# Performance work log

Hardware: AMD Instinct MI355X
Metric: run time of the kernel (lower is better)

The kernel has to match this reference:

```python
import jax, jax.numpy as jnp
import numpy as np

KERNEL_SIZE = 5
SMOOTH_NR = 0.0
SMOOTH_DR = 1e-05


def _box_mean(x, k):
    # Depthwise 3D box (mean) filter via three separable 1-D convolutions.
    # x: [B, C, H, W, D]; zero padding 'SAME' matches F.conv3d(padding=(k-1)//2).
    C = x.shape[1]
    pad = (k - 1) // 2
    for axis in range(3):
        kshape = [1, 1, 1]
        kshape[axis] = k
        kern = jnp.full((C, 1) + tuple(kshape), 1.0 / k, dtype=x.dtype)
        padding = [(pad, pad) if i == axis else (0, 0) for i in range(3)]
        x = jax.lax.conv_general_dilated(
            x, kern, window_strides=(1, 1, 1), padding=padding,
            feature_group_count=C,
            dimension_numbers=('NCDHW', 'OIDHW', 'NCDHW'))
    return x


def setup_inputs() -> dict:
    key = jax.random.key(0)
    k1, k2 = jax.random.split(key)
    shape = (2, 1, 192, 192, 192)
    pred = jax.random.normal(k1, shape, dtype=jnp.float32)
    target = jax.random.normal(k2, shape, dtype=jnp.float32)
    return {"pred": pred, "target": target}


def reference(pred, target):
    k = KERNEL_SIZE
    # Local (windowed) means of the 5 intermediates: I, J, I^2, J^2, I*J.
    # Stack into a single 5C-channel tensor like ffo.create_intermediates,
    # then one grouped box filter (as in the original conv3d with groups=5C).
    C = pred.shape[1]
    interm = jnp.concatenate(
        [pred, target, pred * pred, target * target, pred * target], axis=1)
    m = _box_mean(interm, k)
    uI, uJ, I2, J2, IJ = jnp.split(m, 5, axis=1)
    cross = IJ - uI * uJ          # local covariance (mean form)
    var_i = I2 - uI * uI          # local variance of pred
    var_j = J2 - uJ * uJ          # local variance of target
    ncc = (cross * cross + SMOOTH_NR) / (var_i * var_j + SMOOTH_DR)
    # reduction='mean'; loss is negative squared local NCC
    return -jnp.mean(ncc)
```

## Files before the change

### kernel.cpp

```cpp
#include <hip/hip_runtime.h>

#define HH 192
#define WW 192
#define DD 192
#define BB 2
#define WWDD (WW * DD)
#define HCHUNK 40
#define NSLAB 5
#define SLICES (HCHUNK + 4)

#define QROW 272
#define QSIZE (20 * QROW)
#define IJOFF QSIZE
#define IJROW 72
#define BUFSZ (QSIZE + 20 * IJROW)
#define LDS_BYTES (2 * BUFSZ)

__global__ __launch_bounds__(256, 6)
void lncc_fused_kernel(const float* __restrict__ pred,
                       const float* __restrict__ targ,
                       double* __restrict__ acc_out) {
    __shared__ alignas(16) char lds[LDS_BYTES];
    __shared__ float wpart[4];

    const int tx = threadIdx.x, ty = threadIdx.y;
    const int tid = ty * 16 + tx;

    const int d0 = blockIdx.x * 16;
    const int w0 = blockIdx.y * 16;
    const int bz = blockIdx.z;
    const int b  = bz / NSLAB;
    const int h0 = (bz - b * NSLAB) * HCHUNK;
    const int base = b * (HH * WWDD);

    const int k  = tid >> 3;
    const int dx = tid & 7;
    const int sw  = w0 - 2 + k;
    const int sdb = d0 + 2 * dx - 2;
    const bool prod   = (tid < 160);
    const bool row_ok = prod && ((unsigned)sw < (unsigned)WW);
    const bool ok0 = row_ok && (sdb >= 0);
    const bool ok1 = row_ok;
    const bool ok2 = row_ok && (sdb + 5 < DD);
    const int  gofs = base + sw * DD + sdb;
    char* const qW  = lds + (k * QROW + dx * 32);
    char* const ijW = lds + (IJOFF + k * IJROW + dx * 8);

    const char* const qR  = lds + (ty * QROW + tx * 16);
    const char* const ijR = lds + (IJOFF + ty * IJROW + tx * 4);

    float ring[5][5];
    float hs0 = 0.f, hs1 = 0.f, hs2 = 0.f, hs3 = 0.f, hs4 = 0.f;
#pragma unroll
    for (int q = 0; q < 5; ++q)
#pragma unroll
        for (int i = 0; i < 5; ++i) ring[q][i] = 0.f;
    float acc = 0.f;

    float2 P0, P1, P2, T0, T1, T2;
    auto load_slice = [&](int h) {
        P0 = P1 = P2 = T0 = T1 = T2 = make_float2(0.f, 0.f);
        if ((unsigned)h < (unsigned)HH) {
            const float* pp = pred + (gofs + h * WWDD);
            const float* tt = targ + (gofs + h * WWDD);
            if (ok0) { P0 = *(const float2*)pp;       T0 = *(const float2*)tt; }
            if (ok1) { P1 = *(const float2*)(pp + 2); T1 = *(const float2*)(tt + 2); }
            if (ok2) { P2 = *(const float2*)(pp + 4); T2 = *(const float2*)(tt + 4); }
        }
    };

    load_slice(h0 - 2);

#pragma unroll 2
    for (int it = 0; it < SLICES; ++it) {
        const int buf = (it & 1) * BUFSZ;

        if (prod) {
            const float p0 = P0.x, p1 = P0.y, p2 = P1.x, p3 = P1.y, p4 = P2.x, p5 = P2.y;
            const float q0 = T0.x, q1 = T0.y, q2 = T1.x, q3 = T1.y, q4 = T2.x, q5 = T2.y;
            const float ea0 = p0 + p1 + p2 + p3 + p4,             eb0 = ea0 - p0 + p5;
            const float ea1 = q0 + q1 + q2 + q3 + q4,             eb1 = ea1 - q0 + q5;
            const float pp0 = p0 * p0, pp5 = p5 * p5;
            const float qq0 = q0 * q0, qq5 = q5 * q5;
            const float pq0 = p0 * q0, pq5 = p5 * q5;
            const float ea2 = pp0 + p1*p1 + p2*p2 + p3*p3 + p4*p4, eb2 = ea2 - pp0 + pp5;
            const float ea3 = qq0 + q1*q1 + q2*q2 + q3*q3 + q4*q4, eb3 = ea3 - qq0 + qq5;
            const float ea4 = pq0 + p1*q1 + p2*q2 + p3*q3 + p4*q4, eb4 = ea4 - pq0 + pq5;
            *(float4*)(qW + buf)      = make_float4(ea0, ea1, ea2, ea3);
            *(float4*)(qW + buf + 16) = make_float4(eb0, eb1, eb2, eb3);
            *(float2*)(ijW + buf)     = make_float2(ea4, eb4);
        }

        if (it + 1 < SLICES) load_slice(h0 - 1 + it);

        __syncthreads();

        const char* rq = qR + buf;
        const float4 Q0 = *(const float4*)(rq);
        const float4 Q1 = *(const float4*)(rq + QROW);
        const float4 Q2 = *(const float4*)(rq + 2 * QROW);
        const float4 Q3 = *(const float4*)(rq + 3 * QROW);
        const float4 Q4 = *(const float4*)(rq + 4 * QROW);
        const char* ri = ijR + buf;
        const float An0 = Q0.x + Q1.x + Q2.x + Q3.x + Q4.x;
        const float An1 = Q0.y + Q1.y + Q2.y + Q3.y + Q4.y;
        const float An2 = Q0.z + Q1.z + Q2.z + Q3.z + Q4.z;
        const float An3 = Q0.w + Q1.w + Q2.w + Q3.w + Q4.w;
        const float An4 = *(const float*)(ri)
                        + *(const float*)(ri + IJROW)
                        + *(const float*)(ri + 2 * IJROW)
                        + *(const float*)(ri + 3 * IJROW)
                        + *(const float*)(ri + 4 * IJROW);

        hs0 += An0 - ring[0][0];
        hs1 += An1 - ring[1][0];
        hs2 += An2 - ring[2][0];
        hs3 += An3 - ring[3][0];
        hs4 += An4 - ring[4][0];
#pragma unroll
        for (int q = 0; q < 5; ++q)
#pragma unroll
            for (int i = 0; i < 4; ++i) ring[q][i] = ring[q][i + 1];
        ring[0][4] = An0; ring[1][4] = An1; ring[2][4] = An2;
        ring[3][4] = An3; ring[4][4] = An4;

        if (it >= 4) {
            const int hout = h0 + it - 4;
            if (hout < HH) {
                const float inv = 1.0f / 125.0f;
                const float uI = hs0 * inv, uJ = hs1 * inv;
                const float I2 = hs2 * inv, J2 = hs3 * inv, IJ = hs4 * inv;
                const float cross = IJ - uI * uJ;
                const float vi = I2 - uI * uI;
                const float vj = J2 - uJ * uJ;
                acc += (cross * cross) * __builtin_amdgcn_rcpf(vi * vj + 1e-5f);
            }
        }
    }

#pragma unroll
    for (int off = 32; off > 0; off >>= 1) acc += __shfl_down(acc, off, 64);
    const int wid = tid >> 6, lane = tid & 63;
    if (lane == 0) wpart[wid] = acc;
    __syncthreads();
    if (tid == 0)
        atomicAdd(acc_out, (double)(wpart[0] + wpart[1] + wpart[2] + wpart[3]));
}

__global__ void lncc_finalize_kernel(const double* __restrict__ acc,
                                     float* __restrict__ out) {
    const double n = (double)BB * HH * WW * DD;
    out[0] = (float)(-acc[0] / n);
}

extern "C" void kernel_launch(void* const* d_in, const int* in_sizes, int n_in,
                              void* d_out, int out_size, void* d_ws, size_t ws_size,
                              hipStream_t stream) {
    const float* pred = (const float*)d_in[0];
    const float* targ = (const float*)d_in[1];
    float* out = (float*)d_out;
    double* acc = (double*)d_ws;

    hipMemsetAsync(d_ws, 0, sizeof(double), stream);

    dim3 grid(DD / 16, WW / 16, BB * NSLAB);
    dim3 block(16, 16, 1);
    lncc_fused_kernel<<<grid, block, 0, stream>>>(pred, targ, acc);
    lncc_finalize_kernel<<<1, 1, 0, stream>>>(acc, out);
}
```

Baseline: 186.1 us.

## Replace LDS W-axis box sum with DPP row shifts and drop barriers

The W-direction 5-tap sum now runs inside each wavefront with DPP row-shift operations, where it used to go through double-buffered shared memory behind a __syncthreads every slice. Each lane handles 8 W rows (4 outputs plus halo), so no producer-only thread subset is needed. The H ring buffer is indexed modulo 5 in a 5-way unrolled loop instead of shifting, and HCHUNK changes to 41 so the slice count divides by 5. Block indices are also remapped with an XCD-aware swizzle. The change removes LDS traffic and barriers, but every lane now loads halo data, so global loads are duplicated and the DPP boundary handling must be right.

```diff
diff --git a/kernel.cpp b/kernel.cpp
--- a/kernel.cpp
+++ b/kernel.cpp
@@ -1,61 +1,61 @@
 #include <hip/hip_runtime.h>
+
 
 #define HH 192
 #define WW 192
 #define DD 192
 #define BB 2
 #define WWDD (WW * DD)
-#define HCHUNK 40
+#define HCHUNK 41
 #define NSLAB 5
 #define SLICES (HCHUNK + 4)
+#define GX 12
+#define GY 12
+#define GZ (BB * NSLAB)
+#define NBLK (GX * GY * GZ)
 
-#define QROW 272
-#define QSIZE (20 * QROW)
-#define IJOFF QSIZE
-#define IJROW 72
-#define BUFSZ (QSIZE + 20 * IJROW)
-#define LDS_BYTES (2 * BUFSZ)
+template <int CTRL>
+__device__ __forceinline__ float dpp_f(float x) {
+    union { float f; int i; } a, r;
+    a.f = x;
+    r.i = __builtin_amdgcn_update_dpp(0, a.i, CTRL, 0xF, 0xF, true);
+    return r.f;
+}
 
 __global__ __launch_bounds__(256, 6)
 void lncc_fused_kernel(const float* __restrict__ pred,
                        const float* __restrict__ targ,
                        double* __restrict__ acc_out) {
-    __shared__ alignas(16) char lds[LDS_BYTES];
     __shared__ float wpart[4];
 
-    const int tx = threadIdx.x, ty = threadIdx.y;
-    const int tid = ty * 16 + tx;
+    int flat = blockIdx.x + GX * (blockIdx.y + GY * blockIdx.z);
+    flat = (flat & 7) * (NBLK / 8) + (flat >> 3);
+    const int bx  = flat % GX;
+    const int byz = flat / GX;
+    const int by  = byz % GY;
+    const int bz  = byz / GY;
 
-    const int d0 = blockIdx.x * 16;
-    const int w0 = blockIdx.y * 16;
-    const int bz = blockIdx.z;
+    const int tid  = threadIdx.x;
+    const int wid  = tid >> 6;
+    const int lane = tid & 63;
+    const int rj = lane & 7;
+    const int dx = lane >> 3;
+
+    const int d0 = bx * 16;
+    const int w0 = by * 16;
     const int b  = bz / NSLAB;
     const int h0 = (bz - b * NSLAB) * HCHUNK;
     const int base = b * (HH * WWDD);
 
-    const int k  = tid >> 3;
-    const int dx = tid & 7;
-    const int sw  = w0 - 2 + k;
+    const int ty_base = w0 + 4 * wid;
+    const int sw  = ty_base - 2 + rj;
     const int sdb = d0 + 2 * dx - 2;
-    const bool prod   = (tid < 160);
-    const bool row_ok = prod && ((unsigned)sw < (unsigned)WW);
+    const bool row_ok = ((unsigned)sw < (unsigned)WW);
     const bool ok0 = row_ok && (sdb >= 0);
     const bool ok1 = row_ok;
     const bool ok2 = row_ok && (sdb + 5 < DD);
     const int  gofs = base + sw * DD + sdb;
-    char* const qW  = lds + (k * QROW + dx * 32);
-    char* const ijW = lds + (IJOFF + k * IJROW + dx * 8);
-
-    const char* const qR  = lds + (ty * QROW + tx * 16);
-    const char* const ijR = lds + (IJOFF + ty * IJROW + tx * 4);
-
-    float ring[5][5];
-    float hs0 = 0.f, hs1 = 0.f, hs2 = 0.f, hs3 = 0.f, hs4 = 0.f;
-#pragma unroll
-    for (int q = 0; q < 5; ++q)
-#pragma unroll
-        for (int i = 0; i < 5; ++i) ring[q][i] = 0.f;
-    float acc = 0.f;
+    const bool hi = (rj >= 4);
 
     float2 P0, P1, P2, T0, T1, T2;
     auto load_slice = [&](int h) {
@@ -69,78 +69,71 @@
         }
     };
 
-    load_slice(h0 - 2);
+    float ring[5][5];
+#pragma unroll
+    for (int q = 0; q < 5; ++q)
+#pragma unroll
+        for (int i = 0; i < 5; ++i) ring[q][i] = 0.f;
+    float hs[5] = {0.f, 0.f, 0.f, 0.f, 0.f};
+    float acc = 0.f;
 
-#pragma unroll 2
-    for (int it = 0; it < SLICES; ++it) {
-        const int buf = (it & 1) * BUFSZ;
+#pragma unroll 1
+    for (int mm = 0; mm < SLICES / 5; ++mm) {
+#pragma unroll
+        for (int u = 0; u < 5; ++u) {
+            const int it = 5 * mm + u;
+            load_slice(h0 - 2 + it);
 
-        if (prod) {
-            const float p0 = P0.x, p1 = P0.y, p2 = P1.x, p3 = P1.y, p4 = P2.x, p5 = P2.y;
-            const float q0 = T0.x, q1 = T0.y, q2 = T1.x, q3 = T1.y, q4 = T2.x, q5 = T2.y;
-            const float ea0 = p0 + p1 + p2 + p3 + p4,             eb0 = ea0 - p0 + p5;
-            const float ea1 = q0 + q1 + q2 + q3 + q4,             eb1 = ea1 - q0 + q5;
-            const float pp0 = p0 * p0, pp5 = p5 * p5;
-            const float qq0 = q0 * q0, qq5 = q5 * q5;
-            const float pq0 = p0 * q0, pq5 = p5 * q5;
-            const float ea2 = pp0 + p1*p1 + p2*p2 + p3*p3 + p4*p4, eb2 = ea2 - pp0 + pp5;
-            const float ea3 = qq0 + q1*q1 + q2*q2 + q3*q3 + q4*q4, eb3 = ea3 - qq0 + qq5;
-            const float ea4 = pq0 + p1*q1 + p2*q2 + p3*q3 + p4*q4, eb4 = ea4 - pq0 + pq5;
-            *(float4*)(qW + buf)      = make_float4(ea0, ea1, ea2, ea3);
-            *(float4*)(qW + buf + 16) = make_float4(eb0, eb1, eb2, eb3);
-            *(float2*)(ijW + buf)     = make_float2(ea4, eb4);
-        }
+            const float p0=P0.x, p1=P0.y, p2=P1.x, p3=P1.y, p4=P2.x, p5=P2.y;
+            const float q0=T0.x, q1=T0.y, q2=T1.x, q3=T1.y, q4=T2.x, q5=T2.y;
+            float ea[5], eb[5];
+            ea[0] = p0+p1+p2+p3+p4;  eb[0] = ea[0]-p0+p5;
+            ea[1] = q0+q1+q2+q3+q4;  eb[1] = ea[1]-q0+q5;
+            const float pp0=p0*p0, pp5=p5*p5;
+            const float qq0=q0*q0, qq5=q5*q5;
+            const float pq0=p0*q0, pq5=p5*q5;
+            ea[2] = pp0+p1*p1+p2*p2+p3*p3+p4*p4;  eb[2] = ea[2]-pp0+pp5;
+            ea[3] = qq0+q1*q1+q2*q2+q3*q3+q4*q4;  eb[3] = ea[3]-qq0+qq5;
+            ea[4] = pq0+p1*q1+p2*q2+p3*q3+p4*q4;  eb[4] = ea[4]-pq0+pq5;
 
-        if (it + 1 < SLICES) load_slice(h0 - 1 + it);
+            float An[5];
+#pragma unroll
+            for (int q = 0; q < 5; ++q) {
+                const float va = ea[q], vb = eb[q];
+                float sa = va + dpp_f<0x101>(va);
+                sa = sa + dpp_f<0x102>(sa);
+                const float Wa = sa + dpp_f<0x104>(va);
+                float sb = vb + dpp_f<0x101>(vb);
+                sb = sb + dpp_f<0x102>(sb);
+                const float Wb = sb + dpp_f<0x104>(vb);
+                const float Wbs = dpp_f<0x114>(Wb);
+                An[q] = hi ? Wbs : Wa;
+            }
 
-        __syncthreads();
+#pragma unroll
+            for (int q = 0; q < 5; ++q) {
+                hs[q] += An[q] - ring[q][u];
+                ring[q][u] = An[q];
+            }
 
-        const char* rq = qR + buf;
-        const float4 Q0 = *(const float4*)(rq);
-        const float4 Q1 = *(const float4*)(rq + QROW);
-        const float4 Q2 = *(const float4*)(rq + 2 * QROW);
-        const float4 Q3 = *(const float4*)(rq + 3 * QROW);
-        const float4 Q4 = *(const float4*)(rq + 4 * QROW);
-        const char* ri = ijR + buf;
-        const float An0 = Q0.x + Q1.x + Q2.x + Q3.x + Q4.x;
-        const float An1 = Q0.y + Q1.y + Q2.y + Q3.y + Q4.y;
-        const float An2 = Q0.z + Q1.z + Q2.z + Q3.z + Q4.z;
-        const float An3 = Q0.w + Q1.w + Q2.w + Q3.w + Q4.w;
-        const float An4 = *(const float*)(ri)
-                        + *(const float*)(ri + IJROW)
-                        + *(const float*)(ri + 2 * IJROW)
-                        + *(const float*)(ri + 3 * IJROW)
-                        + *(const float*)(ri + 4 * IJROW);
-
-        hs0 += An0 - ring[0][0];
-        hs1 += An1 - ring[1][0];
-        hs2 += An2 - ring[2][0];
-        hs3 += An3 - ring[3][0];
-        hs4 += An4 - ring[4][0];
-#pragma unroll
-        for (int q = 0; q < 5; ++q)
-#pragma unroll
-            for (int i = 0; i < 4; ++i) ring[q][i] = ring[q][i + 1];
-        ring[0][4] = An0; ring[1][4] = An1; ring[2][4] = An2;
-        ring[3][4] = An3; ring[4][4] = An4;
-
-        if (it >= 4) {
-            const int hout = h0 + it - 4;
-            if (hout < HH) {
-                const float inv = 1.0f / 125.0f;
-                const float uI = hs0 * inv, uJ = hs1 * inv;
-                const float I2 = hs2 * inv, J2 = hs3 * inv, IJ = hs4 * inv;
-                const float cross = IJ - uI * uJ;
-                const float vi = I2 - uI * uI;
-                const float vj = J2 - uJ * uJ;
-                acc += (cross * cross) * __builtin_amdgcn_rcpf(vi * vj + 1e-5f);
+            if (it >= 4) {
+                const int hout = h0 + it - 4;
+                if (hout < HH) {
+                    const float inv = 1.0f / 125.0f;
+                    const float uI = hs[0]*inv, uJ = hs[1]*inv;
+                    const float I2 = hs[2]*inv, J2 = hs[3]*inv, IJ = hs[4]*inv;
+                    const float cross = IJ - uI * uJ;
+                    const float vi = I2 - uI * uI;
+                    const float vj = J2 - uJ * uJ;
+                    acc += (cross * cross) *
+                           __builtin_amdgcn_rcpf(vi * vj + 1e-5f);
+                }
             }
         }
     }
 
 #pragma unroll
     for (int off = 32; off > 0; off >>= 1) acc += __shfl_down(acc, off, 64);
-    const int wid = tid >> 6, lane = tid & 63;
     if (lane == 0) wpart[wid] = acc;
     __syncthreads();
     if (tid == 0)
@@ -163,8 +156,8 @@
 
     hipMemsetAsync(d_ws, 0, sizeof(double), stream);
 
-    dim3 grid(DD / 16, WW / 16, BB * NSLAB);
-    dim3 block(16, 16, 1);
+    dim3 grid(GX, GY, GZ);
+    dim3 block(256, 1, 1);
     lncc_fused_kernel<<<grid, block, 0, stream>>>(pred, targ, acc);
     lncc_finalize_kernel<<<1, 1, 0, stream>>>(acc, out);
 }
```

Measured after the change: 281.8 us. 51.4% more time.

## Give each consumer thread two W-rows, shrink block to 192, swizzle block order

Applied to the files above, without the earlier changes.

The block shrinks from 256 to 192 threads. 160 threads produce the D-direction partial sums and 128 threads consume them, each consumer computing two adjacent W outputs with a sliding-window reuse of the shared LDS rows. The H-ring is unrolled by 5 so ring indexing becomes static instead of shifting registers, and HCHUNK is raised to 41 so the slice count divides by 5. Block indices are remapped so consecutive launches land on spread-out tiles. This cuts consumer LDS reads and register shuffling, at the cost of higher register pressure, lower occupancy bounds and idle producer/consumer lanes.

```diff
diff --git a/kernel.cpp b/kernel.cpp
--- a/kernel.cpp
+++ b/kernel.cpp
@@ -1,13 +1,18 @@
 #include <hip/hip_runtime.h>
+
 
 #define HH 192
 #define WW 192
 #define DD 192
 #define BB 2
 #define WWDD (WW * DD)
-#define HCHUNK 40
+#define HCHUNK 41
 #define NSLAB 5
 #define SLICES (HCHUNK + 4)
+#define GX 12
+#define GY 12
+#define GZ (BB * NSLAB)
+#define NBLK (GX * GY * GZ)
 
 #define QROW 272
 #define QSIZE (20 * QROW)
@@ -16,19 +21,24 @@
 #define BUFSZ (QSIZE + 20 * IJROW)
 #define LDS_BYTES (2 * BUFSZ)
 
-__global__ __launch_bounds__(256, 6)
+__global__ __launch_bounds__(192, 4)
 void lncc_fused_kernel(const float* __restrict__ pred,
                        const float* __restrict__ targ,
                        double* __restrict__ acc_out) {
     __shared__ alignas(16) char lds[LDS_BYTES];
-    __shared__ float wpart[4];
-
-    const int tx = threadIdx.x, ty = threadIdx.y;
-    const int tid = ty * 16 + tx;
-
-    const int d0 = blockIdx.x * 16;
-    const int w0 = blockIdx.y * 16;
-    const int bz = blockIdx.z;
+    __shared__ float wpart[3];
+
+    int flat = blockIdx.x + GX * (blockIdx.y + GY * blockIdx.z);
+    flat = (flat & 7) * (NBLK / 8) + (flat >> 3);
+    const int bx  = flat % GX;
+    const int byz = flat / GX;
+    const int by  = byz % GY;
+    const int bz  = byz / GY;
+
+    const int tid = threadIdx.x;
+
+    const int d0 = bx * 16;
+    const int w0 = by * 16;
     const int b  = bz / NSLAB;
     const int h0 = (bz - b * NSLAB) * HCHUNK;
     const int base = b * (HH * WWDD);
@@ -46,15 +56,23 @@
     char* const qW  = lds + (k * QROW + dx * 32);
     char* const ijW = lds + (IJOFF + k * IJROW + dx * 8);
 
-    const char* const qR  = lds + (ty * QROW + tx * 16);
-    const char* const ijR = lds + (IJOFF + ty * IJROW + tx * 4);
-
-    float ring[5][5];
-    float hs0 = 0.f, hs1 = 0.f, hs2 = 0.f, hs3 = 0.f, hs4 = 0.f;
-#pragma unroll
-    for (int q = 0; q < 5; ++q)
-#pragma unroll
-        for (int i = 0; i < 5; ++i) ring[q][i] = 0.f;
+    const int tx = tid & 15;
+    const int ty = (tid >> 4) & 7;
+    const bool cons = (tid < 128);
+    const char* const qR  = lds + (2 * ty * QROW + tx * 16);
+    const char* const ijR = lds + (IJOFF + 2 * ty * IJROW + tx * 4);
+
+    float ring[2][5][5];
+    float hs[2][5];
+#pragma unroll
+    for (int w01 = 0; w01 < 2; ++w01) {
+#pragma unroll
+        for (int q = 0; q < 5; ++q) {
+            hs[w01][q] = 0.f;
+#pragma unroll
+            for (int i = 0; i < 5; ++i) ring[w01][q][i] = 0.f;
+        }
+    }
     float acc = 0.f;
 
     float2 P0, P1, P2, T0, T1, T2;
@@ -71,69 +89,95 @@
 
     load_slice(h0 - 2);
 
-#pragma unroll 2
-    for (int it = 0; it < SLICES; ++it) {
-        const int buf = (it & 1) * BUFSZ;
-
-        if (prod) {
-            const float p0 = P0.x, p1 = P0.y, p2 = P1.x, p3 = P1.y, p4 = P2.x, p5 = P2.y;
-            const float q0 = T0.x, q1 = T0.y, q2 = T1.x, q3 = T1.y, q4 = T2.x, q5 = T2.y;
-            const float ea0 = p0 + p1 + p2 + p3 + p4,             eb0 = ea0 - p0 + p5;
-            const float ea1 = q0 + q1 + q2 + q3 + q4,             eb1 = ea1 - q0 + q5;
-            const float pp0 = p0 * p0, pp5 = p5 * p5;
-            const float qq0 = q0 * q0, qq5 = q5 * q5;
-            const float pq0 = p0 * q0, pq5 = p5 * q5;
-            const float ea2 = pp0 + p1*p1 + p2*p2 + p3*p3 + p4*p4, eb2 = ea2 - pp0 + pp5;
-            const float ea3 = qq0 + q1*q1 + q2*q2 + q3*q3 + q4*q4, eb3 = ea3 - qq0 + qq5;
-            const float ea4 = pq0 + p1*q1 + p2*q2 + p3*q3 + p4*q4, eb4 = ea4 - pq0 + pq5;
-            *(float4*)(qW + buf)      = make_float4(ea0, ea1, ea2, ea3);
-            *(float4*)(qW + buf + 16) = make_float4(eb0, eb1, eb2, eb3);
-            *(float2*)(ijW + buf)     = make_float2(ea4, eb4);
-        }
-
-        if (it + 1 < SLICES) load_slice(h0 - 1 + it);
-
-        __syncthreads();
-
-        const char* rq = qR + buf;
-        const float4 Q0 = *(const float4*)(rq);
-        const float4 Q1 = *(const float4*)(rq + QROW);
-        const float4 Q2 = *(const float4*)(rq + 2 * QROW);
-        const float4 Q3 = *(const float4*)(rq + 3 * QROW);
-        const float4 Q4 = *(const float4*)(rq + 4 * QROW);
-        const char* ri = ijR + buf;
-        const float An0 = Q0.x + Q1.x + Q2.x + Q3.x + Q4.x;
-        const float An1 = Q0.y + Q1.y + Q2.y + Q3.y + Q4.y;
-        const float An2 = Q0.z + Q1.z + Q2.z + Q3.z + Q4.z;
-        const float An3 = Q0.w + Q1.w + Q2.w + Q3.w + Q4.w;
-        const float An4 = *(const float*)(ri)
-                        + *(const float*)(ri + IJROW)
-                        + *(const float*)(ri + 2 * IJROW)
-                        + *(const float*)(ri + 3 * IJROW)
-                        + *(const float*)(ri + 4 * IJROW);
-
-        hs0 += An0 - ring[0][0];
-        hs1 += An1 - ring[1][0];
-        hs2 += An2 - ring[2][0];
-        hs3 += An3 - ring[3][0];
-        hs4 += An4 - ring[4][0];
-#pragma unroll
-        for (int q = 0; q < 5; ++q)
-#pragma unroll
-            for (int i = 0; i < 4; ++i) ring[q][i] = ring[q][i + 1];
-        ring[0][4] = An0; ring[1][4] = An1; ring[2][4] = An2;
-        ring[3][4] = An3; ring[4][4] = An4;
-
-        if (it >= 4) {
-            const int hout = h0 + it - 4;
-            if (hout < HH) {
-                const float inv = 1.0f / 125.0f;
-                const float uI = hs0 * inv, uJ = hs1 * inv;
-                const float I2 = hs2 * inv, J2 = hs3 * inv, IJ = hs4 * inv;
-                const float cross = IJ - uI * uJ;
-                const float vi = I2 - uI * uI;
-                const float vj = J2 - uJ * uJ;
-                acc += (cross * cross) * __builtin_amdgcn_rcpf(vi * vj + 1e-5f);
+#pragma unroll 1
+    for (int mm = 0; mm < SLICES / 5; ++mm) {
+#pragma unroll
+        for (int u = 0; u < 5; ++u) {
+            const int it = 5 * mm + u;
+            const int buf = (it & 1) * BUFSZ;
+
+            if (prod) {
+                const float p0 = P0.x, p1 = P0.y, p2 = P1.x, p3 = P1.y, p4 = P2.x, p5 = P2.y;
+                const float q0 = T0.x, q1 = T0.y, q2 = T1.x, q3 = T1.y, q4 = T2.x, q5 = T2.y;
+                const float ea0 = p0 + p1 + p2 + p3 + p4,             eb0 = ea0 - p0 + p5;
+                const float ea1 = q0 + q1 + q2 + q3 + q4,             eb1 = ea1 - q0 + q5;
+                const float pp0 = p0 * p0, pp5 = p5 * p5;
+                const float qq0 = q0 * q0, qq5 = q5 * q5;
+                const float pq0 = p0 * q0, pq5 = p5 * q5;
+                const float ea2 = pp0 + p1*p1 + p2*p2 + p3*p3 + p4*p4, eb2 = ea2 - pp0 + pp5;
+                const float ea3 = qq0 + q1*q1 + q2*q2 + q3*q3 + q4*q4, eb3 = ea3 - qq0 + qq5;
+                const float ea4 = pq0 + p1*q1 + p2*q2 + p3*q3 + p4*q4, eb4 = ea4 - pq0 + pq5;
+                *(float4*)(qW + buf)      = make_float4(ea0, ea1, ea2, ea3);
+                *(float4*)(qW + buf + 16) = make_float4(eb0, eb1, eb2, eb3);
+                *(float2*)(ijW + buf)     = make_float2(ea4, eb4);
+            }
+
+            if (it + 1 < SLICES) load_slice(h0 - 1 + it);
+
+            __syncthreads();
+
+            if (cons) {
+                const char* rq = qR + buf;
+                const float4 Q0 = *(const float4*)(rq);
+                const float4 Q1 = *(const float4*)(rq + QROW);
+                const float4 Q2 = *(const float4*)(rq + 2 * QROW);
+                const float4 Q3 = *(const float4*)(rq + 3 * QROW);
+                const float4 Q4 = *(const float4*)(rq + 4 * QROW);
+                const float4 Q5 = *(const float4*)(rq + 5 * QROW);
+                const char* ri = ijR + buf;
+                const float I0 = *(const float*)(ri);
+                const float I1 = *(const float*)(ri + IJROW);
+                const float I2 = *(const float*)(ri + 2 * IJROW);
+                const float I3 = *(const float*)(ri + 3 * IJROW);
+                const float I4 = *(const float*)(ri + 4 * IJROW);
+                const float I5 = *(const float*)(ri + 5 * IJROW);
+
+                const float Ae0 = Q0.x + Q1.x + Q2.x + Q3.x + Q4.x;
+                const float Ae1 = Q0.y + Q1.y + Q2.y + Q3.y + Q4.y;
+                const float Ae2 = Q0.z + Q1.z + Q2.z + Q3.z + Q4.z;
+                const float Ae3 = Q0.w + Q1.w + Q2.w + Q3.w + Q4.w;
+                const float Ae4 = I0 + I1 + I2 + I3 + I4;
+                const float Ao0 = Ae0 - Q0.x + Q5.x;
+                const float Ao1 = Ae1 - Q0.y + Q5.y;
+                const float Ao2 = Ae2 - Q0.z + Q5.z;
+                const float Ao3 = Ae3 - Q0.w + Q5.w;
+                const float Ao4 = Ae4 - I0 + I5;
+
+                hs[0][0] += Ae0 - ring[0][0][u];  ring[0][0][u] = Ae0;
+                hs[0][1] += Ae1 - ring[0][1][u];  ring[0][1][u] = Ae1;
+                hs[0][2] += Ae2 - ring[0][2][u];  ring[0][2][u] = Ae2;
+                hs[0][3] += Ae3 - ring[0][3][u];  ring[0][3][u] = Ae3;
+                hs[0][4] += Ae4 - ring[0][4][u];  ring[0][4][u] = Ae4;
+                hs[1][0] += Ao0 - ring[1][0][u];  ring[1][0][u] = Ao0;
+                hs[1][1] += Ao1 - ring[1][1][u];  ring[1][1][u] = Ao1;
+                hs[1][2] += Ao2 - ring[1][2][u];  ring[1][2][u] = Ao2;
+                hs[1][3] += Ao3 - ring[1][3][u];  ring[1][3][u] = Ao3;
+                hs[1][4] += Ao4 - ring[1][4][u];  ring[1][4][u] = Ao4;
+
+                if (it >= 4) {
+                    const int hout = h0 + it - 4;
+                    if (hout < HH) {
+                        const float inv = 1.0f / 125.0f;
+                        {
+                            const float uI = hs[0][0]*inv, uJ = hs[0][1]*inv;
+                            const float i2 = hs[0][2]*inv, j2 = hs[0][3]*inv, ij = hs[0][4]*inv;
+                            const float cross = ij - uI * uJ;
+                            const float vi = i2 - uI * uI;
+                            const float vj = j2 - uJ * uJ;
+                            acc += (cross * cross) *
+                                   __builtin_amdgcn_rcpf(vi * vj + 1e-5f);
+                        }
+                        {
+                            const float uI = hs[1][0]*inv, uJ = hs[1][1]*inv;
+                            const float i2 = hs[1][2]*inv, j2 = hs[1][3]*inv, ij = hs[1][4]*inv;
+                            const float cross = ij - uI * uJ;
+                            const float vi = i2 - uI * uI;
+                            const float vj = j2 - uJ * uJ;
+                            acc += (cross * cross) *
+                                   __builtin_amdgcn_rcpf(vi * vj + 1e-5f);
+                        }
+                    }
+                }
             }
         }
     }
@@ -144,7 +188,7 @@
     if (lane == 0) wpart[wid] = acc;
     __syncthreads();
     if (tid == 0)
-        atomicAdd(acc_out, (double)(wpart[0] + wpart[1] + wpart[2] + wpart[3]));
+        atomicAdd(acc_out, (double)(wpart[0] + wpart[1] + wpart[2]));
 }
 
 __global__ void lncc_finalize_kernel(const double* __restrict__ acc,
@@ -163,8 +207,8 @@
 
     hipMemsetAsync(d_ws, 0, sizeof(double), stream);
 
-    dim3 grid(DD / 16, WW / 16, BB * NSLAB);
-    dim3 block(16, 16, 1);
+    dim3 grid(GX, GY, GZ);
+    dim3 block(192, 1, 1);
     lncc_fused_kernel<<<grid, block, 0, stream>>>(pred, targ, acc);
     lncc_finalize_kernel<<<1, 1, 0, stream>>>(acc, out);
 }
```

Result: slower. 207.4 us (+11.4%).

## Unroll height loop by five with index-based ring and swizzle block order

Applied to the files above, without the earlier changes.

The height loop is unrolled by five so the five-slot ring buffer is indexed by the unroll position rather than shifted every iteration, which removes register moves. HCHUNK becomes 41 so SLICES (45) divides evenly by five; slabs now cover 205 rows and the hout<HH guard discards the extra rows, adding some redundant work. Block IDs are remapped with a stride-8 swizzle, likely to spread neighbouring tiles across XCDs or caches, and the IJ row pitch is padded from 72 to 76 bytes, likely to change LDS bank mapping.

```diff
diff --git a/kernel.cpp b/kernel.cpp
--- a/kernel.cpp
+++ b/kernel.cpp
@@ -1,18 +1,23 @@
 #include <hip/hip_runtime.h>
+
 
 #define HH 192
 #define WW 192
 #define DD 192
 #define BB 2
 #define WWDD (WW * DD)
-#define HCHUNK 40
+#define HCHUNK 41
 #define NSLAB 5
 #define SLICES (HCHUNK + 4)
+#define GX 12
+#define GY 12
+#define GZ (BB * NSLAB)
+#define NBLK (GX * GY * GZ)
 
 #define QROW 272
 #define QSIZE (20 * QROW)
 #define IJOFF QSIZE
-#define IJROW 72
+#define IJROW 76
 #define BUFSZ (QSIZE + 20 * IJROW)
 #define LDS_BYTES (2 * BUFSZ)
 
@@ -23,12 +28,18 @@
     __shared__ alignas(16) char lds[LDS_BYTES];
     __shared__ float wpart[4];
 
+    int flat = blockIdx.x + GX * (blockIdx.y + GY * blockIdx.z);
+    flat = (flat & 7) * (NBLK / 8) + (flat >> 3);
+    const int bx  = flat % GX;
+    const int byz = flat / GX;
+    const int by  = byz % GY;
+    const int bz  = byz / GY;
+
     const int tx = threadIdx.x, ty = threadIdx.y;
     const int tid = ty * 16 + tx;
 
-    const int d0 = blockIdx.x * 16;
-    const int w0 = blockIdx.y * 16;
-    const int bz = blockIdx.z;
+    const int d0 = bx * 16;
+    const int w0 = by * 16;
     const int b  = bz / NSLAB;
     const int h0 = (bz - b * NSLAB) * HCHUNK;
     const int base = b * (HH * WWDD);
@@ -71,69 +82,67 @@
 
     load_slice(h0 - 2);
 
-#pragma unroll 2
-    for (int it = 0; it < SLICES; ++it) {
-        const int buf = (it & 1) * BUFSZ;
+#pragma unroll 1
+    for (int mm = 0; mm < SLICES / 5; ++mm) {
+#pragma unroll
+        for (int u = 0; u < 5; ++u) {
+            const int it = 5 * mm + u;
+            const int buf = (it & 1) * BUFSZ;
 
-        if (prod) {
-            const float p0 = P0.x, p1 = P0.y, p2 = P1.x, p3 = P1.y, p4 = P2.x, p5 = P2.y;
-            const float q0 = T0.x, q1 = T0.y, q2 = T1.x, q3 = T1.y, q4 = T2.x, q5 = T2.y;
-            const float ea0 = p0 + p1 + p2 + p3 + p4,             eb0 = ea0 - p0 + p5;
-            const float ea1 = q0 + q1 + q2 + q3 + q4,             eb1 = ea1 - q0 + q5;
-            const float pp0 = p0 * p0, pp5 = p5 * p5;
-            const float qq0 = q0 * q0, qq5 = q5 * q5;
-            const float pq0 = p0 * q0, pq5 = p5 * q5;
-            const float ea2 = pp0 + p1*p1 + p2*p2 + p3*p3 + p4*p4, eb2 = ea2 - pp0 + pp5;
-            const float ea3 = qq0 + q1*q1 + q2*q2 + q3*q3 + q4*q4, eb3 = ea3 - qq0 + qq5;
-            const float ea4 = pq0 + p1*q1 + p2*q2 + p3*q3 + p4*q4, eb4 = ea4 - pq0 + pq5;
-            *(float4*)(qW + buf)      = make_float4(ea0, ea1, ea2, ea3);
-            *(float4*)(qW + buf + 16) = make_float4(eb0, eb1, eb2, eb3);
-            *(float2*)(ijW + buf)     = make_float2(ea4, eb4);
-        }
+            if (prod) {
+                const float p0 = P0.x, p1 = P0.y, p2 = P1.x, p3 = P1.y, p4 = P2.x, p5 = P2.y;
+                const float q0 = T0.x, q1 = T0.y, q2 = T1.x, q3 = T1.y, q4 = T2.x, q5 = T2.y;
+                const float ea0 = p0 + p1 + p2 + p3 + p4,             eb0 = ea0 - p0 + p5;
+                const float ea1 = q0 + q1 + q2 + q3 + q4,             eb1 = ea1 - q0 + q5;
+                const float pp0 = p0 * p0, pp5 = p5 * p5;
+                const float qq0 = q0 * q0, qq5 = q5 * q5;
+                const float pq0 = p0 * q0, pq5 = p5 * q5;
+                const float ea2 = pp0 + p1*p1 + p2*p2 + p3*p3 + p4*p4, eb2 = ea2 - pp0 + pp5;
+                const float ea3 = qq0 + q1*q1 + q2*q2 + q3*q3 + q4*q4, eb3 = ea3 - qq0 + qq5;
+                const float ea4 = pq0 + p1*q1 + p2*q2 + p3*q3 + p4*q4, eb4 = ea4 - pq0 + pq5;
+                *(float4*)(qW + buf)      = make_float4(ea0, ea1, ea2, ea3);
+                *(float4*)(qW + buf + 16) = make_float4(eb0, eb1, eb2, eb3);
+                *(float2*)(ijW + buf)     = make_float2(ea4, eb4);
+            }
 
-        if (it + 1 < SLICES) load_slice(h0 - 1 + it);
+            if (it + 1 < SLICES) load_slice(h0 - 1 + it);
 
-        __syncthreads();
+            __syncthreads();
 
-        const char* rq = qR + buf;
-        const float4 Q0 = *(const float4*)(rq);
-        const float4 Q1 = *(const float4*)(rq + QROW);
-        const float4 Q2 = *(const float4*)(rq + 2 * QROW);
-        const float4 Q3 = *(const float4*)(rq + 3 * QROW);
-        const float4 Q4 = *(const float4*)(rq + 4 * QROW);
-        const char* ri = ijR + buf;
-        const float An0 = Q0.x + Q1.x + Q2.x + Q3.x + Q4.x;
-        const float An1 = Q0.y + Q1.y + Q2.y + Q3.y + Q4.y;
-        const float An2 = Q0.z + Q1.z + Q2.z + Q3.z + Q4.z;
-        const float An3 = Q0.w + Q1.w + Q2.w + Q3.w + Q4.w;
-        const float An4 = *(const float*)(ri)
-                        + *(const float*)(ri + IJROW)
-                        + *(const float*)(ri + 2 * IJROW)
-                        + *(const float*)(ri + 3 * IJROW)
-                        + *(const float*)(ri + 4 * IJROW);
+            const char* rq = qR + buf;
+            const float4 Q0 = *(const float4*)(rq);
+            const float4 Q1 = *(const float4*)(rq + QROW);
+            const float4 Q2 = *(const float4*)(rq + 2 * QROW);
+            const float4 Q3 = *(const float4*)(rq + 3 * QROW);
+            const float4 Q4 = *(const float4*)(rq + 4 * QROW);
+            const char* ri = ijR + buf;
+            const float An0 = Q0.x + Q1.x + Q2.x + Q3.x + Q4.x;
+            const float An1 = Q0.y + Q1.y + Q2.y + Q3.y + Q4.y;
+            const float An2 = Q0.z + Q1.z + Q2.z + Q3.z + Q4.z;
+            const float An3 = Q0.w + Q1.w + Q2.w + Q3.w + Q4.w;
+            const float An4 = *(const float*)(ri)
+                            + *(const float*)(ri + IJROW)
+                            + *(const float*)(ri + 2 * IJROW)
+                            + *(const float*)(ri + 3 * IJROW)
+                            + *(const float*)(ri + 4 * IJROW);
 
-        hs0 += An0 - ring[0][0];
-        hs1 += An1 - ring[1][0];
-        hs2 += An2 - ring[2][0];
-        hs3 += An3 - ring[3][0];
-        hs4 += An4 - ring[4][0];
-#pragma unroll
-        for (int q = 0; q < 5; ++q)
-#pragma unroll
-            for (int i = 0; i < 4; ++i) ring[q][i] = ring[q][i + 1];
-        ring[0][4] = An0; ring[1][4] = An1; ring[2][4] = An2;
-        ring[3][4] = An3; ring[4][4] = An4;
+            hs0 += An0 - ring[0][u];  ring[0][u] = An0;
+            hs1 += An1 - ring[1][u];  ring[1][u] = An1;
+            hs2 += An2 - ring[2][u];  ring[2][u] = An2;
+            hs3 += An3 - ring[3][u];  ring[3][u] = An3;
+            hs4 += An4 - ring[4][u];  ring[4][u] = An4;
 
-        if (it >= 4) {
-            const int hout = h0 + it - 4;
-            if (hout < HH) {
-                const float inv = 1.0f / 125.0f;
-                const float uI = hs0 * inv, uJ = hs1 * inv;
-                const float I2 = hs2 * inv, J2 = hs3 * inv, IJ = hs4 * inv;
-                const float cross = IJ - uI * uJ;
-                const float vi = I2 - uI * uI;
-                const float vj = J2 - uJ * uJ;
-                acc += (cross * cross) * __builtin_amdgcn_rcpf(vi * vj + 1e-5f);
+            if (it >= 4) {
+                const int hout = h0 + it - 4;
+                if (hout < HH) {
+                    const float inv = 1.0f / 125.0f;
+                    const float uI = hs0 * inv, uJ = hs1 * inv;
+                    const float I2 = hs2 * inv, J2 = hs3 * inv, IJ = hs4 * inv;
+                    const float cross = IJ - uI * uJ;
+                    const float vi = I2 - uI * uI;
+                    const float vj = J2 - uJ * uJ;
+                    acc += (cross * cross) * __builtin_amdgcn_rcpf(vi * vj + 1e-5f);
+                }
             }
         }
     }
@@ -163,7 +172,7 @@
 
     hipMemsetAsync(d_ws, 0, sizeof(double), stream);
 
-    dim3 grid(DD / 16, WW / 16, BB * NSLAB);
+    dim3 grid(GX, GY, GZ);
     dim3 block(16, 16, 1);
     lncc_fused_kernel<<<grid, block, 0, stream>>>(pred, targ, acc);
     lncc_finalize_kernel<<<1, 1, 0, stream>>>(acc, out);
```

Result: slower. 203.1 us (+9.1%).
